# Kernel optimization log

Hardware: AMD Instinct MI355X
Metric: run time of the kernel (lower is better)

The kernel has to match this reference:

```python
import jax, jax.numpy as jnp
import numpy as np

B, L, D, N, H = 4, 1024, 1024, 16, 64  # batch, seq, d_model, n_head, d_head
R = 2 * L  # relative position table length
EPS = 1e-5


def setup_inputs() -> dict:
    key = jax.random.key(0)
    ks = jax.random.split(key, 16)
    s = D ** -0.5
    q = jax.random.normal(ks[0], (B, L, D), jnp.float32)
    k = jax.random.normal(ks[1], (B, L, D), jnp.float32)
    v = jax.random.normal(ks[2], (B, L, D), jnp.float32)
    pos_encodings = jax.random.normal(ks[3], (R, D), jnp.float32)
    padding = jax.random.randint(ks[4], (B, 1, 1, L), 0, 2).astype(bool)
    q_w = jax.random.normal(ks[5], (D, N, H), jnp.float32) * s
    k_w = jax.random.normal(ks[6], (D, N, H), jnp.float32) * s
    k_b = jnp.zeros((N, H), jnp.float32)
    v_w = jax.random.normal(ks[7], (D, N, H), jnp.float32) * s
    v_b = jnp.zeros((N, H), jnp.float32)
    r_w_bias = jax.random.normal(ks[8], (N, 1, H), jnp.float32) * 0.02
    r_r_bias = jax.random.normal(ks[9], (N, 1, H), jnp.float32) * 0.02
    r_kernel = jax.random.normal(ks[10], (N, D, H), jnp.float32) * s
    post_w = jax.random.normal(ks[11], (N, H, D), jnp.float32) * (N * H) ** -0.5
    post_b = jnp.zeros((D,), jnp.float32)
    ln_g = jnp.ones((D,), jnp.float32)
    ln_b = jnp.zeros((D,), jnp.float32)
    return dict(q=q, k=k, v=v, pos_encodings=pos_encodings, padding=padding,
                q_w=q_w, k_w=k_w, k_b=k_b, v_w=v_w, v_b=v_b,
                r_w_bias=r_w_bias, r_r_bias=r_r_bias, r_kernel=r_kernel,
                post_w=post_w, post_b=post_b, ln_g=ln_g, ln_b=ln_b)


def _funnel_attention(q, k, v, pos_encodings, padding, q_w, k_w, k_b, v_w, v_b,
                      r_w_bias, r_r_bias, r_kernel, post_w, post_b, ln_g, ln_b):
    input_q = q
    d_head = q_w.shape[-1]
    scale = d_head ** -0.5
    # head projections, laid out [b, n, l, h]
    qh = jnp.einsum('bld,dnh->bnlh', q, q_w)
    kh = jnp.einsum('bld,dnh->bnlh', k, k_w) + k_b[None, :, None, :]
    vh = jnp.einsum('bld,dnh->bnlh', v, v_w) + v_b[None, :, None, :]
    # content term with r_w_bias
    attn_score = jnp.einsum('bnlh,bnmh->bnlm', qh + r_w_bias[None], kh) * scale
    # relative-position term (rel_shift)
    r = jnp.einsum('rd,ndh->nrh', pos_encodings, r_kernel)  # [n, R, h]
    pos = jnp.einsum('bnlh,nrh->bnlr', qh + r_r_bias[None], r) * scale  # [b,n,L,R]
    b, n, q_len, r_len = pos.shape
    k_len = kh.shape[-2]
    shift = 1 + (q_len != k_len)
    pos = pos.reshape(b, n, r_len, q_len)
    pos = pos[:, :, shift:, :]
    pos = pos.reshape(b, n, q_len, r_len - shift)[..., :k_len]
    attn_score = attn_score + pos
    # key padding mask
    attn_score = attn_score - 1e6 * padding.astype(attn_score.dtype)
    attn_dist = jax.nn.softmax(attn_score, axis=-1)
    out = jnp.einsum('bnlm,bnmh->bnlh', attn_dist, vh)
    attn_out = jnp.einsum('bnlh,nhd->bld', out, post_w) + post_b
    x = input_q + attn_out
    mu = jnp.mean(x, axis=-1, keepdims=True)
    var = jnp.mean(jnp.square(x - mu), axis=-1, keepdims=True)
    return (x - mu) * jax.lax.rsqrt(var + EPS) * ln_g + ln_b


def reference(q, k, v, pos_encodings, padding, q_w, k_w, k_b, v_w, v_b,
              r_w_bias, r_r_bias, r_kernel, post_w, post_b, ln_g, ln_b):
    return _funnel_attention(q, k, v, pos_encodings, padding, q_w, k_w, k_b,
                             v_w, v_b, r_w_bias, r_r_bias, r_kernel,
                             post_w, post_b, ln_g, ln_b)
```

## Files before the change

kernel.cpp:

```cpp
#include <hip/hip_runtime.h>
#include <hip/hip_bf16.h>

#define Bb 4
#define Ls 1024
#define Dd 1024
#define Nn 16
#define Hh 64
#define Rr 2048

typedef __attribute__((ext_vector_type(8))) short short8;
typedef __attribute__((ext_vector_type(4))) short short4v;
typedef __attribute__((ext_vector_type(4))) float f32x4;

__device__ __forceinline__ float bf2f(short s) {
    union { unsigned u; float f; } c;
    c.u = ((unsigned)(unsigned short)s) << 16;
    return c.f;
}
__device__ __forceinline__ short f2bf(float f) {
    __hip_bfloat16 h = __float2bfloat16(f);
    return *reinterpret_cast<short*>(&h);
}

__device__ __forceinline__ void gld16(const void* g, void* l) {
    __builtin_amdgcn_global_load_lds(
        (const __attribute__((address_space(1))) unsigned int*)g,
        (__attribute__((address_space(3))) unsigned int*)l, 16, 0, 0);
}

struct CopyDesc {
    const float* src[4];
    short* dst[4];
    int n[4];
};
struct TransDesc {
    const float* src[4];
    short* dst[4];
};

__global__ __launch_bounds__(256) void prep_all(
    CopyDesc cd, TransDesc td, const float* __restrict__ rker,
    short* __restrict__ rkT)
{
    const int bid = (int)blockIdx.x;
    const int t   = threadIdx.x;

    if (bid < 8192) {
        const int z = bid >> 11;
        const int base = ((bid & 2047) * 256 + t) * 8;
        if (base >= cd.n[z]) return;
        const float* s = cd.src[z] + base;
        const float4 a = *(const float4*)s;
        const float4 b = *(const float4*)(s + 4);
        short8 o;
        o[0] = f2bf(a.x); o[1] = f2bf(a.y); o[2] = f2bf(a.z); o[3] = f2bf(a.w);
        o[4] = f2bf(b.x); o[5] = f2bf(b.y); o[6] = f2bf(b.z); o[7] = f2bf(b.w);
        *(short8*)(cd.dst[z] + base) = o;
        return;
    }

    const int tw = bid - 8192;
    const float* in; short* out; int C, r0, c0;
    if (tw < 1024) {
        const int z = tw >> 8, rem = tw & 255;
        in = td.src[z]; out = td.dst[z]; C = 1024;
        r0 = ((rem >> 4) & 15) * 64; c0 = (rem & 15) * 64;
    } else {
        const int s2 = tw - 1024;
        const int sl = s2 >> 4, y = s2 & 15;
        in  = rker + (long)sl * 1024 * 64;
        out = rkT  + (long)sl * 64 * 1024;
        C = 64; r0 = y * 64; c0 = 0;
    }
    __shared__ float T[64][65];
    const int rr = t >> 4, c4 = (t & 15) * 4;
#pragma unroll
    for (int p = 0; p < 4; ++p) {
        const float4 v = *(const float4*)&in[(long)(r0 + p * 16 + rr) * C + c0 + c4];
        T[p * 16 + rr][c4 + 0] = v.x;
        T[p * 16 + rr][c4 + 1] = v.y;
        T[p * 16 + rr][c4 + 2] = v.z;
        T[p * 16 + rr][c4 + 3] = v.w;
    }
    __syncthreads();
#pragma unroll
    for (int p = 0; p < 4; ++p) {
        const int j = p * 16 + (t >> 4);
        const int d4 = (t & 15) * 4;
        short4v o;
#pragma unroll
        for (int u = 0; u < 4; ++u) o[u] = f2bf(T[d4 + u][j]);
        *(short4v*)&out[(long)(c0 + j) * 1024 + r0 + d4] = o;
    }
}

__global__ __launch_bounds__(256) void gemm_bt(
    const short* __restrict__ A, int lda, long aStride,
    const short* __restrict__ Bt, int ldb, long bStride,
    const float* __restrict__ bias,
    const float* __restrict__ kb, const float* __restrict__ vb,
    const float* __restrict__ residual, int ldr,
    void* __restrict__ Cv, int ldc, long cStride, int out_bf16, int K, int zsplit)
{
    const int bid   = (int)blockIdx.x;
    const int chunk = (int)gridDim.x >> 3;
    const int work  = (bid & 7) * chunk + (bid >> 3);
    int z, r;
    if (work < zsplit) { z = work >> 8; r = work & 255; }
    else               { z = 3;         r = work - zsplit; }
    const int by = r >> 3;
    const int bx = r & 7;

    A  += (long)z * aStride;
    Bt += (long)z * bStride;

    const int row0 = by * 128;
    const int col0 = bx * 128;

    __shared__ short As[2][128 * 32];
    __shared__ short Bs[2][128 * 32];

    const int tid  = threadIdx.x;
    const int w    = tid >> 6;
    const int lane = tid & 63;
    const int quad = lane >> 4;
    const int ln16 = lane & 15;
    const int wr   = (w >> 1) * 64;
    const int wc   = (w & 1) * 64;

    f32x4 acc[4][4];
#pragma unroll
    for (int a = 0; a < 4; ++a)
#pragma unroll
        for (int b = 0; b < 4; ++b) acc[a][b] = (f32x4){0.f, 0.f, 0.f, 0.f};

    const int srow = w * 16 + (lane >> 2);
    const int scol = (lane & 3) * 8;
    const short* gA = A  + (long)(row0 + srow) * lda + scol;
    const short* gB = Bt + (long)(col0 + srow) * ldb + scol;

    gld16(gA,                  As[0] + w * 512);
    gld16(gA + (long)64 * lda, As[0] + w * 512 + 2048);
    gld16(gB,                  Bs[0] + w * 512);
    gld16(gB + (long)64 * ldb, Bs[0] + w * 512 + 2048);

    int cur = 0;
    for (int k0 = 0; k0 < K; k0 += 32) {
        __builtin_amdgcn_s_barrier();

        if (k0 + 32 < K) {
            const int nxt = cur ^ 1;
            gld16(gA + k0 + 32,                  As[nxt] + w * 512);
            gld16(gA + k0 + 32 + (long)64 * lda, As[nxt] + w * 512 + 2048);
            gld16(gB + k0 + 32,                  Bs[nxt] + w * 512);
            gld16(gB + k0 + 32 + (long)64 * ldb, Bs[nxt] + w * 512 + 2048);
            asm volatile("s_waitcnt vmcnt(4)" ::: "memory");
        } else {
            asm volatile("s_waitcnt vmcnt(0)" ::: "memory");
        }
        __builtin_amdgcn_s_barrier();
        __builtin_amdgcn_sched_barrier(0);

        short8 af[4], bfr[4];
#pragma unroll
        for (int tm = 0; tm < 4; ++tm)
            af[tm] = *(const short8*)&As[cur][(wr + tm * 16 + ln16) * 32 + quad * 8];
#pragma unroll
        for (int tn = 0; tn < 4; ++tn)
            bfr[tn] = *(const short8*)&Bs[cur][(wc + tn * 16 + ln16) * 32 + quad * 8];
#pragma unroll
        for (int tm = 0; tm < 4; ++tm)
#pragma unroll
            for (int tn = 0; tn < 4; ++tn)
                acc[tm][tn] = __builtin_amdgcn_mfma_f32_16x16x32_bf16(
                    af[tm], bfr[tn], acc[tm][tn], 0, 0, 0);

        cur ^= 1;
    }

    const float* bz = bias;
    if (z == 1) bz = kb;
    else if (z == 2) bz = vb;

    float bv[4];
#pragma unroll
    for (int tn = 0; tn < 4; ++tn)
        bv[tn] = bz ? bz[col0 + wc + tn * 16 + ln16] : 0.f;

    short* Cb = (short*)Cv + (long)z * cStride;
    float* Cf = (float*)Cv + (long)z * cStride;
#pragma unroll
    for (int tm = 0; tm < 4; ++tm) {
#pragma unroll
        for (int r2 = 0; r2 < 4; ++r2) {
            const long row = row0 + wr + tm * 16 + quad * 4 + r2;
#pragma unroll
            for (int tn = 0; tn < 4; ++tn) {
                const int col = col0 + wc + tn * 16 + ln16;
                float val = acc[tm][tn][r2] + bv[tn];
                if (residual) val += residual[row * (long)ldr + col];
                if (out_bf16) Cb[row * (long)ldc + col] = f2bf(val);
                else          Cf[row * (long)ldc + col] = val;
            }
        }
    }
}

#define SCALE_L2E 0.18033688f

__global__ __launch_bounds__(256, 2) void attn_mfma(
    const short* __restrict__ qh, const short* __restrict__ kh,
    const short* __restrict__ vh, const short* __restrict__ rS,
    const int* __restrict__ padding, const float* __restrict__ rwb,
    const float* __restrict__ rrb, short* __restrict__ ao)
{
    const int bid   = (int)blockIdx.x;
    const int chunk = (int)gridDim.x >> 3;
    const int work  = (bid & 7) * chunk + (bid >> 3);
    const int lt = work & 7;
    const int n  = (work >> 3) & 15;
    const int b  = work >> 7;

    const int l0 = lt * 128;
    const int tid  = threadIdx.x;
    const int w    = tid >> 6;
    const int lane = tid & 63;
    const int quad = lane >> 4;
    const int ln16 = lane & 15;
    const int qb   = w * 32;

    __shared__ __align__(16) short ks[64 * 64];
    __shared__ __align__(16) short rsb[256 * 64];
    __shared__ __align__(16) short vsT[64][72];
    __shared__ __align__(16) short psm[4][2][16][72];
    __shared__ unsigned padw[32];

#pragma unroll
    for (int j = 0; j < 4; ++j) {
        const int g = w + 4 * j;
        const unsigned long long m =
            __ballot(padding[b * Ls + g * 64 + lane] != 0);
        if (lane == 0) {
            padw[2 * g]     = (unsigned)m;
            padw[2 * g + 1] = (unsigned)(m >> 32);
        }
    }

    short8 qwf[2][2], qrf[2][2];
#pragma unroll
    for (int qt = 0; qt < 2; ++qt) {
        const long rowoff =
            ((long)(b * Ls + l0 + qb + qt * 16 + ln16)) * (Nn * Hh) + n * Hh;
#pragma unroll
        for (int c = 0; c < 2; ++c) {
            const int kb2 = c * 32 + quad * 8;
            short8 qv = *(const short8*)(qh + rowoff + kb2);
#pragma unroll
            for (int j = 0; j < 8; ++j) {
                float qf = bf2f(qv[j]);
                qwf[qt][c][j] = f2bf(qf + rwb[n * Hh + kb2 + j]);
                qrf[qt][c][j] = f2bf(qf + rrb[n * Hh + kb2 + j]);
            }
        }
    }

    float lsum[2][4];
    f32x4 accO[2][4];
#pragma unroll
    for (int qt = 0; qt < 2; ++qt)
#pragma unroll
        for (int r = 0; r < 4; ++r) {
            lsum[qt][r] = 0.f;
            accO[qt][r] = (f32x4){0.f, 0.f, 0.f, 0.f};
        }

    const int srow8 = lane >> 3;
    const int sunit = (lane & 7) ^ srow8;
    const int swz   = ln16 & 7;

    {
        const int base0 = 897 - l0;
#pragma unroll
        for (int j = 0; j < 6; ++j) {
            const int c = w * 6 + j;
            const int rg = base0 + c * 8 + srow8;
            gld16(rS + (long)rg * 1024 + n * 64 + sunit * 8,
                  rsb + c * 512);
        }
    }

    const int s5  = tid & 31;
    const int kp2 = (s5 & 15) + ((s5 >> 4) << 5);
    const int kcb = 4 * (s5 & 15) + 2 * (s5 >> 4);
    const int cq  = (tid >> 5) * 8;
    short8 va, vb2;
    {
        const short* vp = vh + ((long)(b * Ls + kp2)) * 1024 + n * 64 + cq;
        va  = *(const short8*)vp;
        vb2 = *(const short8*)(vp + 16 * 1024);
    }

    for (int mt = 0; mt < Ls / 64; ++mt) {
        const int m0 = mt * 64;
        __syncthreads();

#pragma unroll
        for (int j = 0; j < 2; ++j) {
            const int c = w * 2 + j;
            gld16(kh + ((long)(b * Ls + m0 + c * 8 + srow8)) * 1024
                     + n * 64 + sunit * 8,
                  ks + c * 512);
        }
        {
            const int tail = 1089 + m0 - l0;
            const int rcB  = (24 + 8 * mt) & 31;
#pragma unroll
            for (int j = 0; j < 2; ++j) {
                const int jl = w * 2 + j;
                const int rc = (rcB + jl) & 31;
                int rg = tail + jl * 8 + srow8;
                rg = rg < 2047 ? rg : 2047;
                gld16(rS + (long)rg * 1024 + n * 64 + sunit * 8,
                      rsb + rc * 512);
            }
        }
#pragma unroll
        for (int u = 0; u < 8; ++u) {
            unsigned pk = ((unsigned)(unsigned short)va[u]) |
                          (((unsigned)(unsigned short)vb2[u]) << 16);
            *(unsigned*)&vsT[cq + u][kcb] = pk;
        }
        __syncthreads();

        {
            const int mn = (m0 + 64) & (Ls - 1);
            const short* vp = vh + ((long)(b * Ls + mn + kp2)) * 1024 + n * 64 + cq;
            va  = *(const short8*)vp;
            vb2 = *(const short8*)(vp + 16 * 1024);
        }

        const int rb0 = (96 - qb) + ln16 + m0;
        short8 rfU[6][2];
#pragma unroll
        for (int s = 0; s < 6; ++s) {
            const int rr2 = (rb0 + s * 16) & 255;
#pragma unroll
            for (int c2 = 0; c2 < 2; ++c2) {
                const int unit = (c2 * 4 + quad) ^ swz;
                rfU[s][c2] = *(const short8*)&rsb[rr2 * 64 + unit * 8];
            }
        }

        __builtin_amdgcn_s_setprio(1);
        f32x4 Sf[2][4];
#pragma unroll
        for (int t = 0; t < 4; ++t) {
            short8 kf0, kf1;
            {
                const int u0 = (0 * 4 + quad) ^ swz;
                const int u1 = (1 * 4 + quad) ^ swz;
                kf0 = *(const short8*)&ks[(t * 16 + ln16) * 64 + u0 * 8];
                kf1 = *(const short8*)&ks[(t * 16 + ln16) * 64 + u1 * 8];
            }
#pragma unroll
            for (int qt = 0; qt < 2; ++qt) {
                f32x4 c = (f32x4){0.f, 0.f, 0.f, 0.f};
                c = __builtin_amdgcn_mfma_f32_16x16x32_bf16(qwf[qt][0], kf0, c, 0, 0, 0);
                c = __builtin_amdgcn_mfma_f32_16x16x32_bf16(qwf[qt][1], kf1, c, 0, 0, 0);
                Sf[qt][t] = c;
            }
        }
        f32x4 Prf[2][5];
#pragma unroll
        for (int t = 0; t < 5; ++t) {
#pragma unroll
            for (int qt = 0; qt < 2; ++qt) {
                const int off = qt ? 0 : 1;
                f32x4 c = (f32x4){0.f, 0.f, 0.f, 0.f};
                c = __builtin_amdgcn_mfma_f32_16x16x32_bf16(qrf[qt][0], rfU[t + off][0], c, 0, 0, 0);
                c = __builtin_amdgcn_mfma_f32_16x16x32_bf16(qrf[qt][1], rfU[t + off][1], c, 0, 0, 0);
                Prf[qt][t] = c;
            }
        }
        __builtin_amdgcn_s_setprio(0);

        const unsigned w0 = padw[(m0 >> 5)];
        const unsigned w1 = padw[(m0 >> 5) + 1];
        const float mbc = -16.0f * 1.44269504f;
        const float mb0 = ((w0 >> ln16) & 1)        ? -1.0e7f : mbc;
        const float mb1 = ((w0 >> (16 + ln16)) & 1) ? -1.0e7f : mbc;
        const float mb2 = ((w1 >> ln16) & 1)        ? -1.0e7f : mbc;
        const float mb3 = ((w1 >> (16 + ln16)) & 1) ? -1.0e7f : mbc;
#pragma unroll
        for (int qt = 0; qt < 2; ++qt) {
#pragma unroll
            for (int r = 0; r < 4; ++r) {
                const int row = quad * 4 + r;
                const int u = ln16 - row + 15;
                const int srcLane = (quad << 4) | (u & 15);
                const float s0 = __shfl(Prf[qt][0][r], srcLane, 64);
                const float s1 = __shfl(Prf[qt][1][r], srcLane, 64);
                const float s2 = __shfl(Prf[qt][2][r], srcLane, 64);
                const float s3 = __shfl(Prf[qt][3][r], srcLane, 64);
                const float s4 = __shfl(Prf[qt][4][r], srcLane, 64);
                const bool hi = (u >= 16);
                const float p0 = __builtin_amdgcn_exp2f(
                    fmaf(Sf[qt][0][r] + (hi ? s1 : s0), SCALE_L2E, mb0));
                const float p1 = __builtin_amdgcn_exp2f(
                    fmaf(Sf[qt][1][r] + (hi ? s2 : s1), SCALE_L2E, mb1));
                const float p2 = __builtin_amdgcn_exp2f(
                    fmaf(Sf[qt][2][r] + (hi ? s3 : s2), SCALE_L2E, mb2));
                const float p3 = __builtin_amdgcn_exp2f(
                    fmaf(Sf[qt][3][r] + (hi ? s4 : s3), SCALE_L2E, mb3));
                lsum[qt][r] += (p0 + p1) + (p2 + p3);
                short4v pk;
                pk[0] = f2bf(p0); pk[1] = f2bf(p1);
                pk[2] = f2bf(p2); pk[3] = f2bf(p3);
                *(short4v*)&psm[w][qt][row][ln16 * 4] = pk;
            }
        }

        short8 pA[2][2];
#pragma unroll
        for (int qt = 0; qt < 2; ++qt)
#pragma unroll
            for (int c2 = 0; c2 < 2; ++c2)
                pA[qt][c2] = *(short8*)&psm[w][qt][ln16][c2 * 32 + quad * 8];
        __builtin_amdgcn_s_setprio(1);
#pragma unroll
        for (int t = 0; t < 4; ++t) {
            short8 vf0 = *(short8*)&vsT[t * 16 + ln16][quad * 8];
            short8 vf1 = *(short8*)&vsT[t * 16 + ln16][32 + quad * 8];
#pragma unroll
            for (int qt = 0; qt < 2; ++qt) {
                f32x4 c = accO[qt][t];
                c = __builtin_amdgcn_mfma_f32_16x16x32_bf16(pA[qt][0], vf0, c, 0, 0, 0);
                c = __builtin_amdgcn_mfma_f32_16x16x32_bf16(pA[qt][1], vf1, c, 0, 0, 0);
                accO[qt][t] = c;
            }
        }
        __builtin_amdgcn_s_setprio(0);
    }

#pragma unroll
    for (int qt = 0; qt < 2; ++qt) {
#pragma unroll
        for (int r = 0; r < 4; ++r) {
            float v = lsum[qt][r];
#pragma unroll
            for (int of = 1; of < 16; of <<= 1) v += __shfl_xor(v, of, 64);
            lsum[qt][r] = 1.f / v;
        }
#pragma unroll
        for (int t = 0; t < 4; ++t)
#pragma unroll
            for (int r = 0; r < 4; ++r)
                psm[w][qt][quad * 4 + r][t * 16 + ln16] =
                    f2bf(accO[qt][t][r] * lsum[qt][(unsigned)r]);
#pragma unroll
        for (int p = 0; p < 2; ++p) {
            const int c = lane + p * 64;
            const int row = c >> 3, cq2 = (c & 7) * 8;
            const long grow = (long)(b * Ls + l0 + qb + qt * 16 + row);
            *(short8*)(ao + grow * 1024 + n * 64 + cq2) = *(short8*)&psm[w][qt][row][cq2];
        }
    }
}

__global__ __launch_bounds__(256) void ln_kernel(
    float* x, const float* __restrict__ g, const float* __restrict__ bb)
{
    const int row = blockIdx.x;
    const int tid = threadIdx.x;
    float4 v = ((const float4*)(x + (long)row * Dd))[tid];
    float s  = v.x + v.y + v.z + v.w;
    float sq = v.x * v.x + v.y * v.y + v.z * v.z + v.w * v.w;
#pragma unroll
    for (int off = 32; off; off >>= 1) {
        s  += __shfl_down(s, off, 64);
        sq += __shfl_down(sq, off, 64);
    }
    __shared__ float ws_s[4], ws_q[4];
    __shared__ float s_mu, s_rstd;
    const int wave = tid >> 6, lane = tid & 63;
    if (lane == 0) { ws_s[wave] = s; ws_q[wave] = sq; }
    __syncthreads();
    if (tid == 0) {
        const float ts = ws_s[0] + ws_s[1] + ws_s[2] + ws_s[3];
        const float tq = ws_q[0] + ws_q[1] + ws_q[2] + ws_q[3];
        const float mu = ts / (float)Dd;
        const float var = tq / (float)Dd - mu * mu;
        s_mu = mu;
        s_rstd = rsqrtf(var + 1e-5f);
    }
    __syncthreads();
    const float mu = s_mu, rstd = s_rstd;
    const float4 gv = ((const float4*)g)[tid];
    const float4 bv = ((const float4*)bb)[tid];
    float4 o;
    o.x = (v.x - mu) * rstd * gv.x + bv.x;
    o.y = (v.y - mu) * rstd * gv.y + bv.y;
    o.z = (v.z - mu) * rstd * gv.z + bv.z;
    o.w = (v.w - mu) * rstd * gv.w + bv.w;
    ((float4*)(x + (long)row * Dd))[tid] = o;
}

extern "C" void kernel_launch(void* const* d_in, const int* in_sizes, int n_in,
                              void* d_out, int out_size, void* d_ws, size_t ws_size,
                              hipStream_t stream) {
    const float* q      = (const float*)d_in[0];
    const float* k      = (const float*)d_in[1];
    const float* v      = (const float*)d_in[2];
    const float* posenc = (const float*)d_in[3];
    const int*   pad    = (const int*)  d_in[4];
    const float* q_w    = (const float*)d_in[5];
    const float* k_w    = (const float*)d_in[6];
    const float* k_b    = (const float*)d_in[7];
    const float* v_w    = (const float*)d_in[8];
    const float* v_b    = (const float*)d_in[9];
    const float* rwb    = (const float*)d_in[10];
    const float* rrb    = (const float*)d_in[11];
    const float* r_ker  = (const float*)d_in[12];
    const float* post_w = (const float*)d_in[13];
    const float* post_b = (const float*)d_in[14];
    const float* ln_g   = (const float*)d_in[15];
    const float* ln_b   = (const float*)d_in[16];
    float* out = (float*)d_out;

    const long M1 = 1L << 20;
    short* ws = (short*)d_ws;
    short* xq   = ws;
    short* xk   = ws + 4 * M1;
    short* xv   = ws + 8 * M1;
    short* pe   = ws + 12 * M1;
    short* wT   = ws + 14 * M1;
    short* rkT  = ws + 17 * M1;
    short* pwT  = ws + 18 * M1;
    short* qh   = ws + 19 * M1;
    short* kh   = ws + 23 * M1;
    short* vh   = ws + 27 * M1;
    short* rS   = ws + 31 * M1;
    short* ao   = xq;

    const dim3 blk(256);

    CopyDesc cd;
    cd.src[0] = q;      cd.dst[0] = xq;  cd.n[0] = 4 * (int)M1;
    cd.src[1] = k;      cd.dst[1] = xk;  cd.n[1] = 4 * (int)M1;
    cd.src[2] = v;      cd.dst[2] = xv;  cd.n[2] = 4 * (int)M1;
    cd.src[3] = posenc; cd.dst[3] = pe;  cd.n[3] = 2 * (int)M1;
    TransDesc td;
    td.src[0] = q_w;    td.dst[0] = wT;
    td.src[1] = k_w;    td.dst[1] = wT + M1;
    td.src[2] = v_w;    td.dst[2] = wT + 2 * M1;
    td.src[3] = post_w; td.dst[3] = pwT;
    prep_all<<<dim3(9472), blk, 0, stream>>>(cd, td, r_ker, rkT);

    gemm_bt<<<dim3(896), blk, 0, stream>>>(
        xq, 1024, 4 * M1, wT, 1024, M1, nullptr, k_b, v_b,
        nullptr, 0, qh, 1024, 4 * M1, 1, 1024, 768);

    attn_mfma<<<dim3(512), blk, 0, stream>>>(
        qh, kh, vh, rS, pad, rwb, rrb, ao);

    gemm_bt<<<dim3(256), blk, 0, stream>>>(
        ao, 1024, 0, pwT, 1024, 0, post_b, nullptr, nullptr,
        q, 1024, out, 1024, 0, 0, 1024, 1 << 30);

    ln_kernel<<<dim3(Bb * Ls), blk, 0, stream>>>(out, ln_g, ln_b);
}
```

Before: 289.3 us.

## Double GEMM K-tile to 64 with XOR-swizzled LDS layout

The projection GEMM kernel now loads 64-wide K slices per stage instead of 32, halving the number of barrier/wait iterations. The shared-memory tiles are stored with an XOR swizzle on 16-byte units so the wider rows avoid LDS bank conflicts on fragment reads. This doubles LDS usage per block (64 KB total), which may reduce occupancy, and it uses more registers for the fragments.

```diff
diff --git a/kernel.cpp b/kernel.cpp
--- a/kernel.cpp
+++ b/kernel.cpp
@@ -117,8 +117,8 @@
     const int row0 = by * 128;
     const int col0 = bx * 128;
 
-    __shared__ short As[2][128 * 32];
-    __shared__ short Bs[2][128 * 32];
+    __shared__ short As[2][128 * 64];
+    __shared__ short Bs[2][128 * 64];
 
     const int tid  = threadIdx.x;
     const int w    = tid >> 6;
@@ -134,46 +134,68 @@
 #pragma unroll
         for (int b = 0; b < 4; ++b) acc[a][b] = (f32x4){0.f, 0.f, 0.f, 0.f};
 
-    const int srow = w * 16 + (lane >> 2);
-    const int scol = (lane & 3) * 8;
-    const short* gA = A  + (long)(row0 + srow) * lda + scol;
-    const short* gB = Bt + (long)(col0 + srow) * ldb + scol;
-
-    gld16(gA,                  As[0] + w * 512);
-    gld16(gA + (long)64 * lda, As[0] + w * 512 + 2048);
-    gld16(gB,                  Bs[0] + w * 512);
-    gld16(gB + (long)64 * ldb, Bs[0] + w * 512 + 2048);
+    const int srow8 = lane >> 3;
+    const int sunit = (lane & 7) ^ srow8;
+    const int swz   = ln16 & 7;
+
+#pragma unroll
+    for (int j = 0; j < 4; ++j) {
+        const int c = w * 4 + j;
+        gld16(A  + (long)(row0 + c * 8 + srow8) * lda + sunit * 8,
+              As[0] + c * 512);
+        gld16(Bt + (long)(col0 + c * 8 + srow8) * ldb + sunit * 8,
+              Bs[0] + c * 512);
+    }
 
     int cur = 0;
-    for (int k0 = 0; k0 < K; k0 += 32) {
+    for (int k0 = 0; k0 < K; k0 += 64) {
         __builtin_amdgcn_s_barrier();
 
-        if (k0 + 32 < K) {
+        if (k0 + 64 < K) {
             const int nxt = cur ^ 1;
-            gld16(gA + k0 + 32,                  As[nxt] + w * 512);
-            gld16(gA + k0 + 32 + (long)64 * lda, As[nxt] + w * 512 + 2048);
-            gld16(gB + k0 + 32,                  Bs[nxt] + w * 512);
-            gld16(gB + k0 + 32 + (long)64 * ldb, Bs[nxt] + w * 512 + 2048);
-            asm volatile("s_waitcnt vmcnt(4)" ::: "memory");
+#pragma unroll
+            for (int j = 0; j < 4; ++j) {
+                const int c = w * 4 + j;
+                gld16(A  + (long)(row0 + c * 8 + srow8) * lda + k0 + 64 + sunit * 8,
+                      As[nxt] + c * 512);
+                gld16(Bt + (long)(col0 + c * 8 + srow8) * ldb + k0 + 64 + sunit * 8,
+                      Bs[nxt] + c * 512);
+            }
+            asm volatile("s_waitcnt vmcnt(8)" ::: "memory");
         } else {
             asm volatile("s_waitcnt vmcnt(0)" ::: "memory");
         }
         __builtin_amdgcn_s_barrier();
         __builtin_amdgcn_sched_barrier(0);
 
-        short8 af[4], bfr[4];
+        short8 af[4][2], bfr[4][2];
+#pragma unroll
+        for (int tm = 0; tm < 4; ++tm) {
+            const int row = wr + tm * 16 + ln16;
+#pragma unroll
+            for (int kk = 0; kk < 2; ++kk) {
+                const int unit = (kk * 4 + quad) ^ swz;
+                af[tm][kk] = *(const short8*)&As[cur][row * 64 + unit * 8];
+            }
+        }
+#pragma unroll
+        for (int tn = 0; tn < 4; ++tn) {
+            const int row = wc + tn * 16 + ln16;
+#pragma unroll
+            for (int kk = 0; kk < 2; ++kk) {
+                const int unit = (kk * 4 + quad) ^ swz;
+                bfr[tn][kk] = *(const short8*)&Bs[cur][row * 64 + unit * 8];
+            }
+        }
 #pragma unroll
         for (int tm = 0; tm < 4; ++tm)
-            af[tm] = *(const short8*)&As[cur][(wr + tm * 16 + ln16) * 32 + quad * 8];
-#pragma unroll
-        for (int tn = 0; tn < 4; ++tn)
-            bfr[tn] = *(const short8*)&Bs[cur][(wc + tn * 16 + ln16) * 32 + quad * 8];
-#pragma unroll
-        for (int tm = 0; tm < 4; ++tm)
-#pragma unroll
-            for (int tn = 0; tn < 4; ++tn)
+#pragma unroll
+            for (int tn = 0; tn < 4; ++tn) {
                 acc[tm][tn] = __builtin_amdgcn_mfma_f32_16x16x32_bf16(
-                    af[tm], bfr[tn], acc[tm][tn], 0, 0, 0);
+                    af[tm][0], bfr[tn][0], acc[tm][tn], 0, 0, 0);
+                acc[tm][tn] = __builtin_amdgcn_mfma_f32_16x16x32_bf16(
+                    af[tm][1], bfr[tn][1], acc[tm][tn], 0, 0, 0);
+            }
 
         cur ^= 1;
     }
```

After: 277.3 us. 1.04x faster.
